# Performance work log

Hardware: AMD Instinct MI355X
Metric: run time of the kernel (lower is better)

Reference implementation:

```python
import jax, jax.numpy as jnp
import numpy as np

HIDDEN = 128
NUM_LAYERS = 3
N_NODES = 100000
N_EDGES = 400000
NUM_GRAPHS = 2048


def setup_inputs() -> dict:
    key = jax.random.key(0)
    ks = jax.random.split(key, 10)
    x = jax.random.normal(ks[0], (N_NODES, 1), dtype=jnp.float32)
    edge_index = jax.random.randint(ks[1], (2, N_EDGES), 0, N_NODES, dtype=jnp.int64)
    batch = jnp.sort(jax.random.randint(ks[2], (N_NODES,), 0, NUM_GRAPHS, dtype=jnp.int64))
    s = 1.0 / np.sqrt(HIDDEN)
    W_in = jax.random.normal(ks[3], (1, HIDDEN), dtype=jnp.float32) * s
    b_in = jnp.zeros((HIDDEN,), dtype=jnp.float32)
    W_convs = jax.random.normal(ks[4], (NUM_LAYERS, HIDDEN, HIDDEN), dtype=jnp.float32) * s
    b_convs = jnp.zeros((NUM_LAYERS, HIDDEN), dtype=jnp.float32)
    W_out = jax.random.normal(ks[5], (HIDDEN, HIDDEN), dtype=jnp.float32) * s
    b_out = jnp.zeros((HIDDEN,), dtype=jnp.float32)
    return {"x": x, "edge_index": edge_index, "batch": batch, "num_graphs": NUM_GRAPHS,
            "W_in": W_in, "b_in": b_in, "W_convs": W_convs, "b_convs": b_convs,
            "W_out": W_out, "b_out": b_out}


def reference(x, edge_index, batch, num_graphs, W_in, b_in, W_convs, b_convs, W_out, b_out):
    n_nodes = x.shape[0]
    src, dst = edge_index[0], edge_index[1]
    # GCN symmetric normalization with self-loops: deg = in-degree + 1
    deg = jax.ops.segment_sum(jnp.ones_like(dst, dtype=x.dtype), dst, num_segments=n_nodes) + 1.0
    dinv = deg ** -0.5  # [N]
    edge_norm = (dinv[src] * dinv[dst])[:, None]  # [E,1]
    self_norm = (dinv * dinv)[:, None]            # [N,1], self-loop weight

    h = jax.nn.relu(x @ W_in + b_in)  # [N,H]
    for l in range(W_convs.shape[0]):
        hw = h @ W_convs[l]  # [N,H]
        agg = jax.ops.segment_sum(edge_norm * hw[src], dst, num_segments=n_nodes)
        h = jax.nn.relu(agg + self_norm * hw + b_convs[l])
        # dropout is identity in eval mode

    # global mean pool over graphs
    sums = jax.ops.segment_sum(h, batch, num_segments=num_graphs)  # [G,H]
    cnt = jax.ops.segment_sum(jnp.ones((n_nodes,), dtype=h.dtype), batch, num_segments=num_graphs)
    g = sums / jnp.maximum(cnt, 1.0)[:, None]
    return jax.nn.relu(g @ W_out + b_out)
```

## Files before the change

### kernel.cpp

```cpp
#include <hip/hip_runtime.h>

#define HID 128

typedef __attribute__((ext_vector_type(8))) short short8;
typedef __attribute__((ext_vector_type(4))) float floatx4;

__device__ __forceinline__ float bflo(unsigned u){ return __uint_as_float(u << 16); }
__device__ __forceinline__ float bfhi(unsigned u){ return __uint_as_float(u & 0xffff0000u); }
__device__ __forceinline__ unsigned packbf2(float a, float b){
  unsigned ua = __float_as_uint(a), ub = __float_as_uint(b);
  ua = (ua + 0x7fffu + ((ua >> 16) & 1u)) >> 16;
  ub = (ub + 0x7fffu + ((ub >> 16) & 1u)) >> 16;
  return (ua & 0xffffu) | ((ub & 0xffffu) << 16);
}
__device__ __forceinline__ short8 as_s8(uint4 v){ short8 r; __builtin_memcpy(&r, &v, 16); return r; }

__global__ __launch_bounds__(256) void k_zero(int* __restrict__ p, int n){
  int i = blockIdx.x*256 + threadIdx.x;
  int n4 = n >> 2;
  if (i < n4) ((int4*)p)[i] = (int4){0,0,0,0};
  if (i == 0) for (int r = n4*4; r < n; ++r) p[r] = 0;
}

__global__ __launch_bounds__(256) void k_deg(const int* __restrict__ dst, int* __restrict__ cnt, int E){
  int e = blockIdx.x*256 + threadIdx.x;
  if (e < E) atomicAdd(&cnt[dst[e]], 1);
}

__global__ __launch_bounds__(1024) void k_scan1(const int* __restrict__ cnt, int* __restrict__ rp,
                                                int* __restrict__ bsum, float* __restrict__ dinv, int N){
  __shared__ int s[1024];
  int t = threadIdx.x;
  int i = blockIdx.x*1024 + t;
  int v = (i < N) ? cnt[i] : 0;
  s[t] = v;
  __syncthreads();
  for (int d = 1; d < 1024; d <<= 1) {
    int add = (t >= d) ? s[t - d] : 0;
    __syncthreads();
    s[t] += add;
    __syncthreads();
  }
  if (i < N) {
    rp[i] = s[t] - v;
    dinv[i] = 1.0f / sqrtf((float)v + 1.0f);
  }
  if (t == 1023) bsum[blockIdx.x] = s[1023];
}

__global__ __launch_bounds__(1024) void k_scan3(int* __restrict__ rp, int* __restrict__ cursor,
                                                const int* __restrict__ bsum, int nb, int N){
  __shared__ int s[128];
  int t = threadIdx.x;
  if (t < 128) s[t] = (t < nb) ? bsum[t] : 0;
  __syncthreads();
  for (int d = 1; d < 128; d <<= 1) {
    int add = 0;
    if (t < 128 && t >= d) add = s[t - d];
    __syncthreads();
    if (t < 128) s[t] += add;
    __syncthreads();
  }
  int base = (blockIdx.x > 0) ? s[blockIdx.x - 1] : 0;
  int i = blockIdx.x*1024 + t;
  if (i < N) {
    int v = rp[i] + base;
    rp[i] = v;
    cursor[i] = v;
  }
  if (blockIdx.x == 0 && t == 0) rp[N] = s[nb - 1];
}

__global__ __launch_bounds__(256) void k_fill(const int* __restrict__ src, const int* __restrict__ dst,
                                              int* __restrict__ cursor, int2* __restrict__ ew,
                                              const float* __restrict__ dinv, int E){
  int e = blockIdx.x*256 + threadIdx.x;
  if (e < E){
    int d = dst[e], s = src[e];
    int pos = atomicAdd(&cursor[d], 1);
    int2 pk; pk.x = s; pk.y = __float_as_int(dinv[s]);
    ew[pos] = pk;
  }
}

__global__ __launch_bounds__(256) void k_prepw(const float* __restrict__ Wc, uint4* __restrict__ wf){
  int t = blockIdx.x*256 + threadIdx.x;
  if (t >= 3*2048) return;
  int l = t >> 11, r = t & 2047;
  int kt = r >> 9, ct = (r >> 6) & 7, lane = r & 63;
  int kbase = kt*32 + (lane >> 4)*8;
  int m = ct*16 + (lane & 15);
  const float* Wl = Wc + l*16384;
  float v[8];
  #pragma unroll
  for (int i = 0; i < 8; ++i) v[i] = Wl[(kbase + i)*128 + m];
  uint4 o;
  o.x = packbf2(v[0], v[1]);
  o.y = packbf2(v[2], v[3]);
  o.z = packbf2(v[4], v[5]);
  o.w = packbf2(v[6], v[7]);
  wf[t] = o;
}

__global__ __launch_bounds__(256) void k_gemm0(const float* __restrict__ x,
                                               const float* __restrict__ Win,
                                               const float* __restrict__ bin,
                                               const uint4* __restrict__ wf,
                                               unsigned short* __restrict__ hwout, int N){
  __shared__ uint4 lwf[2048];
  __shared__ float sw[128], sb[128];
  int t = threadIdx.x;
  #pragma unroll
  for (int j = 0; j < 8; ++j) lwf[t + j*256] = wf[t + j*256];
  if (t < 128) { sw[t] = Win[t]; sb[t] = bin[t]; }
  __syncthreads();
  int lane = t & 63, w = t >> 6;
  int rb = blockIdx.x*128 + w*32;
  int nrow0 = rb + (lane & 15);
  int nrow1 = nrow0 + 16;
  float xv0 = x[nrow0 < N ? nrow0 : N - 1];
  float xv1 = x[nrow1 < N ? nrow1 : N - 1];
  floatx4 acc0[8], acc1[8];
  #pragma unroll
  for (int c = 0; c < 8; ++c) { acc0[c] = (floatx4){0.f,0.f,0.f,0.f}; acc1[c] = (floatx4){0.f,0.f,0.f,0.f}; }
  #pragma unroll
  for (int kt = 0; kt < 4; ++kt) {
    int k0 = kt*32 + (lane >> 4)*8;
    float hv0[8], hv1[8];
    #pragma unroll
    for (int i = 0; i < 8; ++i) {
      float wv = sw[k0 + i], bv = sb[k0 + i];
      hv0[i] = fmaxf(fmaf(xv0, wv, bv), 0.f);
      hv1[i] = fmaxf(fmaf(xv1, wv, bv), 0.f);
    }
    uint4 p0, p1;
    p0.x = packbf2(hv0[0], hv0[1]); p0.y = packbf2(hv0[2], hv0[3]);
    p0.z = packbf2(hv0[4], hv0[5]); p0.w = packbf2(hv0[6], hv0[7]);
    p1.x = packbf2(hv1[0], hv1[1]); p1.y = packbf2(hv1[2], hv1[3]);
    p1.z = packbf2(hv1[4], hv1[5]); p1.w = packbf2(hv1[6], hv1[7]);
    short8 hf0 = as_s8(p0), hf1 = as_s8(p1);
    #pragma unroll
    for (int c = 0; c < 8; ++c) {
      short8 af = as_s8(lwf[(kt*8 + c)*64 + lane]);
      acc0[c] = __builtin_amdgcn_mfma_f32_16x16x32_bf16(af, hf0, acc0[c], 0, 0, 0);
      acc1[c] = __builtin_amdgcn_mfma_f32_16x16x32_bf16(af, hf1, acc1[c], 0, 0, 0);
    }
  }
  if (nrow0 < N) {
    unsigned short* op = hwout + (size_t)nrow0*128 + (lane >> 4)*4;
    #pragma unroll
    for (int c = 0; c < 8; ++c) {
      uint2 pk;
      pk.x = packbf2(acc0[c][0], acc0[c][1]);
      pk.y = packbf2(acc0[c][2], acc0[c][3]);
      *(uint2*)(op + c*16) = pk;
    }
  }
  if (nrow1 < N) {
    unsigned short* op = hwout + (size_t)nrow1*128 + (lane >> 4)*4;
    #pragma unroll
    for (int c = 0; c < 8; ++c) {
      uint2 pk;
      pk.x = packbf2(acc1[c][0], acc1[c][1]);
      pk.y = packbf2(acc1[c][2], acc1[c][3]);
      *(uint2*)(op + c*16) = pk;
    }
  }
}

__global__ __launch_bounds__(256) void k_gemm(const unsigned short* __restrict__ hin,
                                              const uint4* __restrict__ wf,
                                              unsigned short* __restrict__ hwout, int N){
  __shared__ uint4 lwf[2048];
  int t = threadIdx.x;
  #pragma unroll
  for (int j = 0; j < 8; ++j) lwf[t + j*256] = wf[t + j*256];
  __syncthreads();
  int lane = t & 63, w = t >> 6;
  int rb = blockIdx.x*128 + w*32;
  int nrow0 = rb + (lane & 15);
  int nrow1 = nrow0 + 16;
  int nc0 = nrow0 < N ? nrow0 : N - 1;
  int nc1 = nrow1 < N ? nrow1 : N - 1;
  const uint4* hp0 = (const uint4*)(hin + (size_t)nc0*128 + (lane >> 4)*8);
  const uint4* hp1 = (const uint4*)(hin + (size_t)nc1*128 + (lane >> 4)*8);
  floatx4 acc0[8], acc1[8];
  #pragma unroll
  for (int c = 0; c < 8; ++c) { acc0[c] = (floatx4){0.f,0.f,0.f,0.f}; acc1[c] = (floatx4){0.f,0.f,0.f,0.f}; }
  #pragma unroll
  for (int kt = 0; kt < 4; ++kt) {
    short8 hf0 = as_s8(hp0[kt*4]);
    short8 hf1 = as_s8(hp1[kt*4]);
    #pragma unroll
    for (int c = 0; c < 8; ++c) {
      short8 af = as_s8(lwf[(kt*8 + c)*64 + lane]);
      acc0[c] = __builtin_amdgcn_mfma_f32_16x16x32_bf16(af, hf0, acc0[c], 0, 0, 0);
      acc1[c] = __builtin_amdgcn_mfma_f32_16x16x32_bf16(af, hf1, acc1[c], 0, 0, 0);
    }
  }
  if (nrow0 < N) {
    unsigned short* op = hwout + (size_t)nrow0*128 + (lane >> 4)*4;
    #pragma unroll
    for (int c = 0; c < 8; ++c) {
      uint2 pk;
      pk.x = packbf2(acc0[c][0], acc0[c][1]);
      pk.y = packbf2(acc0[c][2], acc0[c][3]);
      *(uint2*)(op + c*16) = pk;
    }
  }
  if (nrow1 < N) {
    unsigned short* op = hwout + (size_t)nrow1*128 + (lane >> 4)*4;
    #pragma unroll
    for (int c = 0; c < 8; ++c) {
      uint2 pk;
      pk.x = packbf2(acc1[c][0], acc1[c][1]);
      pk.y = packbf2(acc1[c][2], acc1[c][3]);
      *(uint2*)(op + c*16) = pk;
    }
  }
}

__global__ __launch_bounds__(256) void k_agg(const uint2* __restrict__ hw2, uint2* __restrict__ h2,
                                             const int* __restrict__ rp, const int2* __restrict__ ew,
                                             const float* __restrict__ dinv,
                                             const float* __restrict__ bias, int N){
  int node = (blockIdx.x * blockDim.x + threadIdx.x) >> 5;
  int c = threadIdx.x & 31;
  if (node >= N) return;
  float dn = dinv[node];
  size_t rbase = (size_t)node * 32;
  uint2 su = hw2[rbase + c];
  float a0 = dn * bflo(su.x), a1 = dn * bfhi(su.x);
  float a2 = dn * bflo(su.y), a3 = dn * bfhi(su.y);
  int e0 = rp[node], e1 = rp[node + 1];
  int last = e1 - 1;
  for (int e = e0; e < e1; e += 4) {
    int i1 = e + 1 <= last ? e + 1 : last;
    int i2 = e + 2 <= last ? e + 2 : last;
    int i3 = e + 3 <= last ? e + 3 : last;
    int2 p0 = ew[e], p1 = ew[i1], p2 = ew[i2], p3 = ew[i3];
    float w0 = __int_as_float(p0.y);
    float w1 = e + 1 <= last ? __int_as_float(p1.y) : 0.f;
    float w2 = e + 2 <= last ? __int_as_float(p2.y) : 0.f;
    float w3 = e + 3 <= last ? __int_as_float(p3.y) : 0.f;
    uint2 v0 = hw2[(size_t)p0.x * 32 + c];
    uint2 v1 = hw2[(size_t)p1.x * 32 + c];
    uint2 v2 = hw2[(size_t)p2.x * 32 + c];
    uint2 v3 = hw2[(size_t)p3.x * 32 + c];
    a0 = fmaf(w0, bflo(v0.x), a0); a1 = fmaf(w0, bfhi(v0.x), a1);
    a2 = fmaf(w0, bflo(v0.y), a2); a3 = fmaf(w0, bfhi(v0.y), a3);
    a0 = fmaf(w1, bflo(v1.x), a0); a1 = fmaf(w1, bfhi(v1.x), a1);
    a2 = fmaf(w1, bflo(v1.y), a2); a3 = fmaf(w1, bfhi(v1.y), a3);
    a0 = fmaf(w2, bflo(v2.x), a0); a1 = fmaf(w2, bfhi(v2.x), a1);
    a2 = fmaf(w2, bflo(v2.y), a2); a3 = fmaf(w2, bfhi(v2.y), a3);
    a0 = fmaf(w3, bflo(v3.x), a0); a1 = fmaf(w3, bfhi(v3.x), a1);
    a2 = fmaf(w3, bflo(v3.y), a2); a3 = fmaf(w3, bfhi(v3.y), a3);
  }
  float4 bv = *(const float4*)(bias + c*4);
  float r0 = fmaxf(fmaf(dn, a0, bv.x), 0.f);
  float r1 = fmaxf(fmaf(dn, a1, bv.y), 0.f);
  float r2 = fmaxf(fmaf(dn, a2, bv.z), 0.f);
  float r3 = fmaxf(fmaf(dn, a3, bv.w), 0.f);
  uint2 o;
  o.x = packbf2(r0, r1);
  o.y = packbf2(r2, r3);
  h2[rbase + c] = o;
}

__global__ __launch_bounds__(256) void k_pool(const uint4* __restrict__ h4, const int* __restrict__ batch,
                                              float* __restrict__ gp, int N, int G){
  int g = blockIdx.x * 4 + (threadIdx.x >> 6);
  int lane = threadIdx.x & 63;
  if (g >= G) return;
  int lo, hi;
  { int a = 0, b = N; while (a < b) { int m = (a + b) >> 1; if (batch[m] < g) a = m + 1; else b = m; } lo = a; }
  { int a = lo, b = N; while (a < b) { int m = (a + b) >> 1; if (batch[m] < g + 1) a = m + 1; else b = m; } hi = a; }
  int r = lane >> 4;
  int c = lane & 15;
  float a0=0.f,a1=0.f,a2=0.f,a3=0.f,a4=0.f,a5=0.f,a6=0.f,a7=0.f;
  for (int n = lo + r; n < hi; n += 4) {
    uint4 v = h4[(size_t)n*16 + c];
    a0 += bflo(v.x); a1 += bfhi(v.x);
    a2 += bflo(v.y); a3 += bfhi(v.y);
    a4 += bflo(v.z); a5 += bfhi(v.z);
    a6 += bflo(v.w); a7 += bfhi(v.w);
  }
  #pragma unroll
  for (int m = 16; m <= 32; m <<= 1) {
    a0 += __shfl_xor(a0, m, 64); a1 += __shfl_xor(a1, m, 64);
    a2 += __shfl_xor(a2, m, 64); a3 += __shfl_xor(a3, m, 64);
    a4 += __shfl_xor(a4, m, 64); a5 += __shfl_xor(a5, m, 64);
    a6 += __shfl_xor(a6, m, 64); a7 += __shfl_xor(a7, m, 64);
  }
  if (r == 0) {
    float inv = 1.0f / fmaxf((float)(hi - lo), 1.0f);
    float4* o = (float4*)(gp + (size_t)g*128 + c*8);
    o[0] = (float4){a0*inv, a1*inv, a2*inv, a3*inv};
    o[1] = (float4){a4*inv, a5*inv, a6*inv, a7*inv};
  }
}

__global__ __launch_bounds__(128) void k_out(const float* __restrict__ gp, const float* __restrict__ Wout,
                                             const float* __restrict__ bout, float* __restrict__ out, int G){
  __shared__ float sg[128];
  int g = blockIdx.x, c = threadIdx.x;
  sg[c] = gp[g*128 + c];
  __syncthreads();
  float a = 0.f;
  #pragma unroll
  for (int k = 0; k < 128; ++k) a = fmaf(sg[k], Wout[k*128 + c], a);
  out[g*128 + c] = fmaxf(a + bout[c], 0.f);
}

extern "C" void kernel_launch(void* const* d_in, const int* in_sizes, int n_in,
                              void* d_out, int out_size, void* d_ws, size_t ws_size,
                              hipStream_t stream){
  (void)n_in; (void)ws_size;
  const float* x       = (const float*)d_in[0];
  const int*   ei      = (const int*)d_in[1];
  const int*   batch   = (const int*)d_in[2];
  const float* W_in    = (const float*)d_in[4];
  const float* b_in    = (const float*)d_in[5];
  const float* W_convs = (const float*)d_in[6];
  const float* b_convs = (const float*)d_in[7];
  const float* W_out   = (const float*)d_in[8];
  const float* b_out   = (const float*)d_in[9];
  float* out = (float*)d_out;

  int N = in_sizes[0];
  int E = in_sizes[1] / 2;
  int G = out_size / HID;

  char* p = (char*)d_ws;
  auto alloc = [&](size_t bytes) -> char* {
    char* r = p; p += (bytes + 255) & ~(size_t)255; return r;
  };
  unsigned* h      = (unsigned*)alloc((size_t)N * 64 * 4);
  unsigned* hw     = (unsigned*)alloc((size_t)N * 64 * 4);
  uint4*    wf     = (uint4*)   alloc(3 * 2048 * 16);
  float*    dinv   = (float*)   alloc((size_t)N * 4);
  int*      cnt    = (int*)     alloc((size_t)N * 4);
  int*      rp     = (int*)     alloc((size_t)(N + 1) * 4);
  int*      cursor = (int*)     alloc((size_t)(N + 1) * 4);
  int2*     ew     = (int2*)    alloc((size_t)E * 8);
  float*    gp     = (float*)   alloc((size_t)G * HID * 4);
  int*      bsum   = (int*)     alloc(4096);

  const int* src  = ei;
  const int* dstp = ei + E;

  k_zero<<<(N/4 + 255) / 256, 256, 0, stream>>>(cnt, N);
  k_deg <<<(E + 255) / 256, 256, 0, stream>>>(dstp, cnt, E);
  int nb = (N + 1023) / 1024;
  k_scan1<<<nb, 1024, 0, stream>>>(cnt, rp, bsum, dinv, N);
  k_scan3<<<nb, 1024, 0, stream>>>(rp, cursor, bsum, nb, N);
  k_fill<<<(E + 255) / 256, 256, 0, stream>>>(src, dstp, cursor, ew, dinv, E);
  k_prepw<<<24, 256, 0, stream>>>(W_convs, wf);

  int gb = (N + 127) / 128;
  k_gemm0<<<gb, 256, 0, stream>>>(x, W_in, b_in, wf, (unsigned short*)hw, N);
  k_agg  <<<(N + 7) / 8, 256, 0, stream>>>((const uint2*)hw, (uint2*)h, rp, ew, dinv, b_convs, N);
  for (int l = 1; l < 3; ++l) {
    k_gemm<<<gb, 256, 0, stream>>>((const unsigned short*)h, wf + l * 2048,
                                   (unsigned short*)hw, N);
    k_agg <<<(N + 7) / 8, 256, 0, stream>>>((const uint2*)hw, (uint2*)h, rp, ew, dinv,
                                            b_convs + l * HID, N);
  }

  k_pool<<<(G + 3) / 4, 256, 0, stream>>>((const uint4*)h, batch, gp, N, G);
  k_out <<<G, HID, 0, stream>>>(gp, W_out, b_out, out, G);
}
```

Baseline: 219.2 us.

## Fuse aggregation of layer l with GEMM of layer l+1 via LDS tile

Replaces separate k_agg and k_gemm launches for the middle layers with a fused kernel. Each block aggregates 128 nodes into a swizzled bf16 tile in shared memory, then runs the MFMA GEMM on that tile. The weights are now read directly from global memory instead of being staged in LDS. This removes the write and re-read of the intermediate h and two kernel launches. The cost is lower gather parallelism per block, since each half-wave now handles 16 nodes serially, and an extra hw ping-pong buffer.

```diff
diff --git a/kernel.cpp b/kernel.cpp
--- a/kernel.cpp
+++ b/kernel.cpp
@@ -168,54 +168,99 @@
   }
 }
 
-__global__ __launch_bounds__(256) void k_gemm(const unsigned short* __restrict__ hin,
-                                              const uint4* __restrict__ wf,
-                                              unsigned short* __restrict__ hwout, int N){
-  __shared__ uint4 lwf[2048];
+__global__ __launch_bounds__(256) void k_fused(const uint2* __restrict__ hw2in,
+                                               const uint4* __restrict__ wf,
+                                               const int* __restrict__ rp, const int2* __restrict__ ew,
+                                               const float* __restrict__ dinv,
+                                               const float* __restrict__ bias,
+                                               unsigned short* __restrict__ hwout, int N){
+  __shared__ __align__(16) unsigned char htile[128*256];
   int t = threadIdx.x;
-  #pragma unroll
-  for (int j = 0; j < 8; ++j) lwf[t + j*256] = wf[t + j*256];
+  int rb = blockIdx.x * 128;
+  int hwid = t >> 5, c = t & 31;
+  for (int it = 0; it < 16; ++it) {
+    int lrow = hwid*16 + it;
+    int node = rb + lrow;
+    if (node < N) {
+      float dn = dinv[node];
+      size_t rbase = (size_t)node * 32;
+      uint2 su = hw2in[rbase + c];
+      float a0 = dn * bflo(su.x), a1 = dn * bfhi(su.x);
+      float a2 = dn * bflo(su.y), a3 = dn * bfhi(su.y);
+      int e0 = rp[node], e1 = rp[node + 1];
+      int last = e1 - 1;
+      for (int e = e0; e < e1; e += 4) {
+        int i1 = e + 1 <= last ? e + 1 : last;
+        int i2 = e + 2 <= last ? e + 2 : last;
+        int i3 = e + 3 <= last ? e + 3 : last;
+        int2 p0 = ew[e], p1 = ew[i1], p2 = ew[i2], p3 = ew[i3];
+        float w0 = __int_as_float(p0.y);
+        float w1 = e + 1 <= last ? __int_as_float(p1.y) : 0.f;
+        float w2 = e + 2 <= last ? __int_as_float(p2.y) : 0.f;
+        float w3 = e + 3 <= last ? __int_as_float(p3.y) : 0.f;
+        uint2 v0 = hw2in[(size_t)p0.x * 32 + c];
+        uint2 v1 = hw2in[(size_t)p1.x * 32 + c];
+        uint2 v2 = hw2in[(size_t)p2.x * 32 + c];
+        uint2 v3 = hw2in[(size_t)p3.x * 32 + c];
+        a0 = fmaf(w0, bflo(v0.x), a0); a1 = fmaf(w0, bfhi(v0.x), a1);
+        a2 = fmaf(w0, bflo(v0.y), a2); a3 = fmaf(w0, bfhi(v0.y), a3);
+        a0 = fmaf(w1, bflo(v1.x), a0); a1 = fmaf(w1, bfhi(v1.x), a1);
+        a2 = fmaf(w1, bflo(v1.y), a2); a3 = fmaf(w1, bfhi(v1.y), a3);
+        a0 = fmaf(w2, bflo(v2.x), a0); a1 = fmaf(w2, bfhi(v2.x), a1);
+        a2 = fmaf(w2, bflo(v2.y), a2); a3 = fmaf(w2, bfhi(v2.y), a3);
+        a0 = fmaf(w3, bflo(v3.x), a0); a1 = fmaf(w3, bfhi(v3.x), a1);
+        a2 = fmaf(w3, bflo(v3.y), a2); a3 = fmaf(w3, bfhi(v3.y), a3);
+      }
+      float4 bv = *(const float4*)(bias + c*4);
+      float r0 = fmaxf(fmaf(dn, a0, bv.x), 0.f);
+      float r1 = fmaxf(fmaf(dn, a1, bv.y), 0.f);
+      float r2 = fmaxf(fmaf(dn, a2, bv.z), 0.f);
+      float r3 = fmaxf(fmaf(dn, a3, bv.w), 0.f);
+      uint2 o;
+      o.x = packbf2(r0, r1);
+      o.y = packbf2(r2, r3);
+      *(uint2*)(&htile[(unsigned)(lrow*256 + c*8) ^ ((lrow & 7u) << 4)]) = o;
+    }
+  }
   __syncthreads();
   int lane = t & 63, w = t >> 6;
-  int rb = blockIdx.x*128 + w*32;
-  int nrow0 = rb + (lane & 15);
-  int nrow1 = nrow0 + 16;
-  int nc0 = nrow0 < N ? nrow0 : N - 1;
-  int nc1 = nrow1 < N ? nrow1 : N - 1;
-  const uint4* hp0 = (const uint4*)(hin + (size_t)nc0*128 + (lane >> 4)*8);
-  const uint4* hp1 = (const uint4*)(hin + (size_t)nc1*128 + (lane >> 4)*8);
+  int lr0 = w*32 + (lane & 15);
+  int lr1 = lr0 + 16;
+  int nrow0 = rb + lr0, nrow1 = rb + lr1;
+  const uint4* wfp = wf + lane;
   floatx4 acc0[8], acc1[8];
   #pragma unroll
-  for (int c = 0; c < 8; ++c) { acc0[c] = (floatx4){0.f,0.f,0.f,0.f}; acc1[c] = (floatx4){0.f,0.f,0.f,0.f}; }
+  for (int cc = 0; cc < 8; ++cc) { acc0[cc] = (floatx4){0.f,0.f,0.f,0.f}; acc1[cc] = (floatx4){0.f,0.f,0.f,0.f}; }
   #pragma unroll
   for (int kt = 0; kt < 4; ++kt) {
-    short8 hf0 = as_s8(hp0[kt*4]);
-    short8 hf1 = as_s8(hp1[kt*4]);
-    #pragma unroll
-    for (int c = 0; c < 8; ++c) {
-      short8 af = as_s8(lwf[(kt*8 + c)*64 + lane]);
-      acc0[c] = __builtin_amdgcn_mfma_f32_16x16x32_bf16(af, hf0, acc0[c], 0, 0, 0);
-      acc1[c] = __builtin_amdgcn_mfma_f32_16x16x32_bf16(af, hf1, acc1[c], 0, 0, 0);
+    uint4 b0 = *(const uint4*)(&htile[(unsigned)(lr0*256 + kt*64 + (lane >> 4)*16) ^ ((lr0 & 7u) << 4)]);
+    uint4 b1 = *(const uint4*)(&htile[(unsigned)(lr1*256 + kt*64 + (lane >> 4)*16) ^ ((lr1 & 7u) << 4)]);
+    short8 hf0 = as_s8(b0), hf1 = as_s8(b1);
+    #pragma unroll
+    for (int cc = 0; cc < 8; ++cc) {
+      short8 af = as_s8(wfp[(kt*8 + cc)*64]);
+      acc0[cc] = __builtin_amdgcn_mfma_f32_16x16x32_bf16(af, hf0, acc0[cc], 0, 0, 0);
+      acc1[cc] = __builtin_amdgcn_mfma_f32_16x16x32_bf16(af, hf1, acc1[cc], 0, 0, 0);
     }
   }
   if (nrow0 < N) {
     unsigned short* op = hwout + (size_t)nrow0*128 + (lane >> 4)*4;
     #pragma unroll
-    for (int c = 0; c < 8; ++c) {
+    for (int cc = 0; cc < 8; ++cc) {
       uint2 pk;
-      pk.x = packbf2(acc0[c][0], acc0[c][1]);
-      pk.y = packbf2(acc0[c][2], acc0[c][3]);
-      *(uint2*)(op + c*16) = pk;
+      pk.x = packbf2(acc0[cc][0], acc0[cc][1]);
+      pk.y = packbf2(acc0[cc][2], acc0[cc][3]);
+      *(uint2*)(op + cc*16) = pk;
     }
   }
   if (nrow1 < N) {
     unsigned short* op = hwout + (size_t)nrow1*128 + (lane >> 4)*4;
     #pragma unroll
-    for (int c = 0; c < 8; ++c) {
+    for (int cc = 0; cc < 8; ++cc) {
       uint2 pk;
-      pk.x = packbf2(acc1[c][0], acc1[c][1]);
-      pk.y = packbf2(acc1[c][2], acc1[c][3]);
-      *(uint2*)(op + c*16) = pk;
+      pk.x = packbf2(acc1[cc][0], acc1[cc][1]);
+      pk.y = packbf2(acc1[cc][2], acc1[cc][3]);
+      *(uint2*)(op + cc*16) = pk;
     }
   }
 }
@@ -336,7 +381,8 @@
     char* r = p; p += (bytes + 255) & ~(size_t)255; return r;
   };
   unsigned* h      = (unsigned*)alloc((size_t)N * 64 * 4);
-  unsigned* hw     = (unsigned*)alloc((size_t)N * 64 * 4);
+  unsigned* hwA    = (unsigned*)alloc((size_t)N * 64 * 4);
+  unsigned* hwB    = (unsigned*)alloc((size_t)N * 64 * 4);
   uint4*    wf     = (uint4*)   alloc(3 * 2048 * 16);
   float*    dinv   = (float*)   alloc((size_t)N * 4);
   int*      cnt    = (int*)     alloc((size_t)N * 4);
@@ -358,14 +404,13 @@
   k_prepw<<<24, 256, 0, stream>>>(W_convs, wf);
 
   int gb = (N + 127) / 128;
-  k_gemm0<<<gb, 256, 0, stream>>>(x, W_in, b_in, wf, (unsigned short*)hw, N);
-  k_agg  <<<(N + 7) / 8, 256, 0, stream>>>((const uint2*)hw, (uint2*)h, rp, ew, dinv, b_convs, N);
-  for (int l = 1; l < 3; ++l) {
-    k_gemm<<<gb, 256, 0, stream>>>((const unsigned short*)h, wf + l * 2048,
-                                   (unsigned short*)hw, N);
-    k_agg <<<(N + 7) / 8, 256, 0, stream>>>((const uint2*)hw, (uint2*)h, rp, ew, dinv,
-                                            b_convs + l * HID, N);
-  }
+  k_gemm0<<<gb, 256, 0, stream>>>(x, W_in, b_in, wf, (unsigned short*)hwA, N);
+  k_fused<<<gb, 256, 0, stream>>>((const uint2*)hwA, wf + 2048, rp, ew, dinv,
+                                  b_convs, (unsigned short*)hwB, N);
+  k_fused<<<gb, 256, 0, stream>>>((const uint2*)hwB, wf + 4096, rp, ew, dinv,
+                                  b_convs + HID, (unsigned short*)hwA, N);
+  k_agg<<<(N + 7) / 8, 256, 0, stream>>>((const uint2*)hwA, (uint2*)h, rp, ew, dinv,
+                                         b_convs + 2*HID, N);
 
   k_pool<<<(G + 3) / 4, 256, 0, stream>>>((const uint4*)h, batch, gp, N, G);
   k_out <<<G, HID, 0, stream>>>(gp, W_out, b_out, out, G);
```

Result: slower. 283.9 us (+29.5%).

## Merge independent launches and fuse pooling with output projection

Applied to the files above, without the earlier changes.

Combines zeroing with weight prep into one launch, runs CSR fill alongside the first GEMM in a single launch, and fuses mean-pool with the output linear layer. The aggregation loop drops index clamping by padding the edge array with four zeroed entries, so the weight-zero tail reads stay in bounds. This removes several kernel launches and the intermediate pooled buffer. The cost is that the fill blocks now share a grid with GEMM blocks that reserve large shared memory.

```diff
diff --git a/kernel.cpp b/kernel.cpp
--- a/kernel.cpp
+++ b/kernel.cpp
@@ -15,11 +15,36 @@
 }
 __device__ __forceinline__ short8 as_s8(uint4 v){ short8 r; __builtin_memcpy(&r, &v, 16); return r; }
 
-__global__ __launch_bounds__(256) void k_zero(int* __restrict__ p, int n){
-  int i = blockIdx.x*256 + threadIdx.x;
-  int n4 = n >> 2;
-  if (i < n4) ((int4*)p)[i] = (int4){0,0,0,0};
-  if (i == 0) for (int r = n4*4; r < n; ++r) p[r] = 0;
+__global__ __launch_bounds__(256) void k_init(int* __restrict__ cnt, int N,
+                                              int2* __restrict__ ew, int E,
+                                              const float* __restrict__ Wc, uint4* __restrict__ wf,
+                                              int zb){
+  if ((int)blockIdx.x < zb) {
+    int i = blockIdx.x*256 + threadIdx.x;
+    int n4 = N >> 2;
+    if (i < n4) ((int4*)cnt)[i] = (int4){0,0,0,0};
+    if (blockIdx.x == 0 && threadIdx.x == 0) {
+      for (int r = n4*4; r < N; ++r) cnt[r] = 0;
+      for (int r = 0; r < 4; ++r) { int2 z; z.x = 0; z.y = 0; ew[E + r] = z; }
+    }
+    return;
+  }
+  int t = ((int)blockIdx.x - zb)*256 + threadIdx.x;
+  if (t >= 3*2048) return;
+  int l = t >> 11, r = t & 2047;
+  int kt = r >> 9, ct = (r >> 6) & 7, lane = r & 63;
+  int kbase = kt*32 + (lane >> 4)*8;
+  int m = ct*16 + (lane & 15);
+  const float* Wl = Wc + l*16384;
+  float v[8];
+  #pragma unroll
+  for (int i = 0; i < 8; ++i) v[i] = Wl[(kbase + i)*128 + m];
+  uint4 o;
+  o.x = packbf2(v[0], v[1]);
+  o.y = packbf2(v[2], v[3]);
+  o.z = packbf2(v[4], v[5]);
+  o.w = packbf2(v[6], v[7]);
+  wf[t] = o;
 }
 
 __global__ __launch_bounds__(256) void k_deg(const int* __restrict__ dst, int* __restrict__ cnt, int E){
@@ -71,51 +96,33 @@
   if (blockIdx.x == 0 && t == 0) rp[N] = s[nb - 1];
 }
 
-__global__ __launch_bounds__(256) void k_fill(const int* __restrict__ src, const int* __restrict__ dst,
-                                              int* __restrict__ cursor, int2* __restrict__ ew,
-                                              const float* __restrict__ dinv, int E){
-  int e = blockIdx.x*256 + threadIdx.x;
-  if (e < E){
-    int d = dst[e], s = src[e];
-    int pos = atomicAdd(&cursor[d], 1);
-    int2 pk; pk.x = s; pk.y = __float_as_int(dinv[s]);
-    ew[pos] = pk;
-  }
-}
-
-__global__ __launch_bounds__(256) void k_prepw(const float* __restrict__ Wc, uint4* __restrict__ wf){
-  int t = blockIdx.x*256 + threadIdx.x;
-  if (t >= 3*2048) return;
-  int l = t >> 11, r = t & 2047;
-  int kt = r >> 9, ct = (r >> 6) & 7, lane = r & 63;
-  int kbase = kt*32 + (lane >> 4)*8;
-  int m = ct*16 + (lane & 15);
-  const float* Wl = Wc + l*16384;
-  float v[8];
-  #pragma unroll
-  for (int i = 0; i < 8; ++i) v[i] = Wl[(kbase + i)*128 + m];
-  uint4 o;
-  o.x = packbf2(v[0], v[1]);
-  o.y = packbf2(v[2], v[3]);
-  o.z = packbf2(v[4], v[5]);
-  o.w = packbf2(v[6], v[7]);
-  wf[t] = o;
-}
-
-__global__ __launch_bounds__(256) void k_gemm0(const float* __restrict__ x,
-                                               const float* __restrict__ Win,
-                                               const float* __restrict__ bin,
-                                               const uint4* __restrict__ wf,
-                                               unsigned short* __restrict__ hwout, int N){
+__global__ __launch_bounds__(256) void k_fill_gemm0(const int* __restrict__ src, const int* __restrict__ dst,
+                                                    int* __restrict__ cursor, int2* __restrict__ ew,
+                                                    const float* __restrict__ dinv, int E, int fb,
+                                                    const float* __restrict__ x,
+                                                    const float* __restrict__ Win,
+                                                    const float* __restrict__ bin,
+                                                    const uint4* __restrict__ wf,
+                                                    unsigned short* __restrict__ hwout, int N){
   __shared__ uint4 lwf[2048];
   __shared__ float sw[128], sb[128];
+  if ((int)blockIdx.x < fb) {
+    int e = blockIdx.x*256 + threadIdx.x;
+    if (e < E){
+      int d = dst[e], s = src[e];
+      int pos = atomicAdd(&cursor[d], 1);
+      int2 pk; pk.x = s; pk.y = __float_as_int(dinv[s]);
+      ew[pos] = pk;
+    }
+    return;
+  }
   int t = threadIdx.x;
   #pragma unroll
   for (int j = 0; j < 8; ++j) lwf[t + j*256] = wf[t + j*256];
   if (t < 128) { sw[t] = Win[t]; sb[t] = bin[t]; }
   __syncthreads();
   int lane = t & 63, w = t >> 6;
-  int rb = blockIdx.x*128 + w*32;
+  int rb = ((int)blockIdx.x - fb)*128 + w*32;
   int nrow0 = rb + (lane & 15);
   int nrow1 = nrow0 + 16;
   float xv0 = x[nrow0 < N ? nrow0 : N - 1];
@@ -233,20 +240,16 @@
   float a0 = dn * bflo(su.x), a1 = dn * bfhi(su.x);
   float a2 = dn * bflo(su.y), a3 = dn * bfhi(su.y);
   int e0 = rp[node], e1 = rp[node + 1];
-  int last = e1 - 1;
   for (int e = e0; e < e1; e += 4) {
-    int i1 = e + 1 <= last ? e + 1 : last;
-    int i2 = e + 2 <= last ? e + 2 : last;
-    int i3 = e + 3 <= last ? e + 3 : last;
-    int2 p0 = ew[e], p1 = ew[i1], p2 = ew[i2], p3 = ew[i3];
-    float w0 = __int_as_float(p0.y);
-    float w1 = e + 1 <= last ? __int_as_float(p1.y) : 0.f;
-    float w2 = e + 2 <= last ? __int_as_float(p2.y) : 0.f;
-    float w3 = e + 3 <= last ? __int_as_float(p3.y) : 0.f;
+    int2 p0 = ew[e], p1 = ew[e+1], p2 = ew[e+2], p3 = ew[e+3];
     uint2 v0 = hw2[(size_t)p0.x * 32 + c];
     uint2 v1 = hw2[(size_t)p1.x * 32 + c];
     uint2 v2 = hw2[(size_t)p2.x * 32 + c];
     uint2 v3 = hw2[(size_t)p3.x * 32 + c];
+    float w0 = __int_as_float(p0.y);
+    float w1 = (e + 1 < e1) ? __int_as_float(p1.y) : 0.f;
+    float w2 = (e + 2 < e1) ? __int_as_float(p2.y) : 0.f;
+    float w3 = (e + 3 < e1) ? __int_as_float(p3.y) : 0.f;
     a0 = fmaf(w0, bflo(v0.x), a0); a1 = fmaf(w0, bfhi(v0.x), a1);
     a2 = fmaf(w0, bflo(v0.y), a2); a3 = fmaf(w0, bfhi(v0.y), a3);
     a0 = fmaf(w1, bflo(v1.x), a0); a1 = fmaf(w1, bfhi(v1.x), a1);
@@ -267,49 +270,53 @@
   h2[rbase + c] = o;
 }
 
-__global__ __launch_bounds__(256) void k_pool(const uint4* __restrict__ h4, const int* __restrict__ batch,
-                                              float* __restrict__ gp, int N, int G){
-  int g = blockIdx.x * 4 + (threadIdx.x >> 6);
+__global__ __launch_bounds__(256) void k_poolout(const uint4* __restrict__ h4, const int* __restrict__ batch,
+                                                 const float* __restrict__ Wout, const float* __restrict__ bout,
+                                                 float* __restrict__ out, int N, int G){
+  __shared__ float sg[4][128];
+  int wv = threadIdx.x >> 6;
+  int g = blockIdx.x * 4 + wv;
   int lane = threadIdx.x & 63;
-  if (g >= G) return;
-  int lo, hi;
-  { int a = 0, b = N; while (a < b) { int m = (a + b) >> 1; if (batch[m] < g) a = m + 1; else b = m; } lo = a; }
-  { int a = lo, b = N; while (a < b) { int m = (a + b) >> 1; if (batch[m] < g + 1) a = m + 1; else b = m; } hi = a; }
-  int r = lane >> 4;
-  int c = lane & 15;
-  float a0=0.f,a1=0.f,a2=0.f,a3=0.f,a4=0.f,a5=0.f,a6=0.f,a7=0.f;
-  for (int n = lo + r; n < hi; n += 4) {
-    uint4 v = h4[(size_t)n*16 + c];
-    a0 += bflo(v.x); a1 += bfhi(v.x);
-    a2 += bflo(v.y); a3 += bfhi(v.y);
-    a4 += bflo(v.z); a5 += bfhi(v.z);
-    a6 += bflo(v.w); a7 += bfhi(v.w);
-  }
-  #pragma unroll
-  for (int m = 16; m <= 32; m <<= 1) {
-    a0 += __shfl_xor(a0, m, 64); a1 += __shfl_xor(a1, m, 64);
-    a2 += __shfl_xor(a2, m, 64); a3 += __shfl_xor(a3, m, 64);
-    a4 += __shfl_xor(a4, m, 64); a5 += __shfl_xor(a5, m, 64);
-    a6 += __shfl_xor(a6, m, 64); a7 += __shfl_xor(a7, m, 64);
-  }
-  if (r == 0) {
-    float inv = 1.0f / fmaxf((float)(hi - lo), 1.0f);
-    float4* o = (float4*)(gp + (size_t)g*128 + c*8);
-    o[0] = (float4){a0*inv, a1*inv, a2*inv, a3*inv};
-    o[1] = (float4){a4*inv, a5*inv, a6*inv, a7*inv};
-  }
-}
-
-__global__ __launch_bounds__(128) void k_out(const float* __restrict__ gp, const float* __restrict__ Wout,
-                                             const float* __restrict__ bout, float* __restrict__ out, int G){
-  __shared__ float sg[128];
-  int g = blockIdx.x, c = threadIdx.x;
-  sg[c] = gp[g*128 + c];
-  __syncthreads();
-  float a = 0.f;
-  #pragma unroll
-  for (int k = 0; k < 128; ++k) a = fmaf(sg[k], Wout[k*128 + c], a);
-  out[g*128 + c] = fmaxf(a + bout[c], 0.f);
+  if (g < G) {
+    int lo, hi;
+    { int a = 0, b = N; while (a < b) { int m = (a + b) >> 1; if (batch[m] < g) a = m + 1; else b = m; } lo = a; }
+    { int a = lo, b = N; while (a < b) { int m = (a + b) >> 1; if (batch[m] < g + 1) a = m + 1; else b = m; } hi = a; }
+    int r = lane >> 4;
+    int c = lane & 15;
+    float a0=0.f,a1=0.f,a2=0.f,a3=0.f,a4=0.f,a5=0.f,a6=0.f,a7=0.f;
+    for (int n = lo + r; n < hi; n += 4) {
+      uint4 v = h4[(size_t)n*16 + c];
+      a0 += bflo(v.x); a1 += bfhi(v.x);
+      a2 += bflo(v.y); a3 += bfhi(v.y);
+      a4 += bflo(v.z); a5 += bfhi(v.z);
+      a6 += bflo(v.w); a7 += bfhi(v.w);
+    }
+    #pragma unroll
+    for (int m = 16; m <= 32; m <<= 1) {
+      a0 += __shfl_xor(a0, m, 64); a1 += __shfl_xor(a1, m, 64);
+      a2 += __shfl_xor(a2, m, 64); a3 += __shfl_xor(a3, m, 64);
+      a4 += __shfl_xor(a4, m, 64); a5 += __shfl_xor(a5, m, 64);
+      a6 += __shfl_xor(a6, m, 64); a7 += __shfl_xor(a7, m, 64);
+    }
+    if (r == 0) {
+      float inv = 1.0f / fmaxf((float)(hi - lo), 1.0f);
+      float* o = &sg[wv][c*8];
+      o[0] = a0*inv; o[1] = a1*inv; o[2] = a2*inv; o[3] = a3*inv;
+      o[4] = a4*inv; o[5] = a5*inv; o[6] = a6*inv; o[7] = a7*inv;
+    }
+  }
+  __syncthreads();
+  if (g < G) {
+    float acc0 = 0.f, acc1 = 0.f;
+    #pragma unroll 4
+    for (int k = 0; k < 128; ++k) {
+      float hv = sg[wv][k];
+      acc0 = fmaf(hv, Wout[k*128 + lane],      acc0);
+      acc1 = fmaf(hv, Wout[k*128 + lane + 64], acc1);
+    }
+    out[(size_t)g*128 + lane]      = fmaxf(acc0 + bout[lane],      0.f);
+    out[(size_t)g*128 + lane + 64] = fmaxf(acc1 + bout[lane + 64], 0.f);
+  }
 }
 
 extern "C" void kernel_launch(void* const* d_in, const int* in_sizes, int n_in,
@@ -342,24 +349,25 @@
   int*      cnt    = (int*)     alloc((size_t)N * 4);
   int*      rp     = (int*)     alloc((size_t)(N + 1) * 4);
   int*      cursor = (int*)     alloc((size_t)(N + 1) * 4);
-  int2*     ew     = (int2*)    alloc((size_t)E * 8);
-  float*    gp     = (float*)   alloc((size_t)G * HID * 4);
+  int2*     ew     = (int2*)    alloc((size_t)(E + 4) * 8);
   int*      bsum   = (int*)     alloc(4096);
 
   const int* src  = ei;
   const int* dstp = ei + E;
 
-  k_zero<<<(N/4 + 255) / 256, 256, 0, stream>>>(cnt, N);
+  int zb = (N/4 + 255) / 256;
+  k_init<<<zb + 24, 256, 0, stream>>>(cnt, N, ew, E, W_convs, wf, zb);
   k_deg <<<(E + 255) / 256, 256, 0, stream>>>(dstp, cnt, E);
   int nb = (N + 1023) / 1024;
   k_scan1<<<nb, 1024, 0, stream>>>(cnt, rp, bsum, dinv, N);
   k_scan3<<<nb, 1024, 0, stream>>>(rp, cursor, bsum, nb, N);
-  k_fill<<<(E + 255) / 256, 256, 0, stream>>>(src, dstp, cursor, ew, dinv, E);
-  k_prepw<<<24, 256, 0, stream>>>(W_convs, wf);
-
+
+  int fb = (E + 255) / 256;
   int gb = (N + 127) / 128;
-  k_gemm0<<<gb, 256, 0, stream>>>(x, W_in, b_in, wf, (unsigned short*)hw, N);
-  k_agg  <<<(N + 7) / 8, 256, 0, stream>>>((const uint2*)hw, (uint2*)h, rp, ew, dinv, b_convs, N);
+  k_fill_gemm0<<<fb + gb, 256, 0, stream>>>(src, dstp, cursor, ew, dinv, E, fb,
+                                            x, W_in, b_in, wf, (unsigned short*)hw, N);
+
+  k_agg <<<(N + 7) / 8, 256, 0, stream>>>((const uint2*)hw, (uint2*)h, rp, ew, dinv, b_convs, N);
   for (int l = 1; l < 3; ++l) {
     k_gemm<<<gb, 256, 0, stream>>>((const unsigned short*)h, wf + l * 2048,
                                    (unsigned short*)hw, N);
@@ -367,6 +375,5 @@
                                             b_convs + l * HID, N);
   }
 
-  k_pool<<<(G + 3) / 4, 256, 0, stream>>>((const uint4*)h, batch, gp, N, G);
-  k_out <<<G, HID, 0, stream>>>(gp, W_out, b_out, out, G);
-}
+  k_poolout<<<(G + 3) / 4, 256, 0, stream>>>((const uint4*)h, batch, W_out, b_out, out, N, G);
+}
```

Measured after the change: 206.8 us. -5.6%, faster.
